# Performance work log

Hardware: AMD Instinct MI355X
Metric: run time of the kernel (lower is better)

Reference implementation:

```python
import jax, jax.numpy as jnp
import numpy as np

B, S, D_MODEL, N_HEADS = 4, 2048, 1024, 16
HEAD = D_MODEL // N_HEADS  # 64


def setup_inputs() -> dict:
    key = jax.random.key(0)
    ks = jax.random.split(key, 9)
    s = 1.0 / np.sqrt(D_MODEL)
    return {
        "query": jax.random.normal(ks[0], (B, S, D_MODEL), jnp.float32),
        "key_in": jax.random.normal(ks[1], (B, S, D_MODEL), jnp.float32),
        "value": jax.random.normal(ks[2], (B, S, D_MODEL), jnp.float32),
        "Wq": jax.random.normal(ks[3], (D_MODEL, D_MODEL), jnp.float32) * s,
        "bq": jnp.zeros((D_MODEL,), jnp.float32),
        "Wk": jax.random.normal(ks[4], (D_MODEL, D_MODEL), jnp.float32) * s,
        "bk": jnp.zeros((D_MODEL,), jnp.float32),
        "Wv": jax.random.normal(ks[5], (D_MODEL, D_MODEL), jnp.float32) * s,
        "bv": jnp.zeros((D_MODEL,), jnp.float32),
    }


def reference(query, key_in, value, Wq, bq, Wk, bk, Wv, bv):
    # Dense projections (Keras Dense: x @ W + b)
    q = query @ Wq + bq     # [B,S,D]
    k = key_in @ Wk + bk    # [B,S,D]
    v = value @ Wv + bv     # [B,S,D]
    # split heads -> [B,S,H,Dh]
    q = q.reshape(B, S, N_HEADS, HEAD)
    k = k.reshape(B, S, N_HEADS, HEAD)
    v = v.reshape(B, S, N_HEADS, HEAD)
    scale = 1.0 / jnp.sqrt(jnp.float32(HEAD))
    # full attention matrix [B,H,Sq,Sk] (faithful to original un-fused form)
    scores = jnp.einsum('bqhd,bkhd->bhqk', q, k) * scale
    alpha = jax.nn.softmax(scores, axis=-1)
    ctx = jnp.einsum('bhqk,bkhd->bqhd', alpha, v)  # [B,Sq,H,Dh]
    return ctx.reshape(B, S, D_MODEL)
```

## Files before the change

kernel.cpp:

```cpp
#include <hip/hip_runtime.h>
#include <hip/hip_bf16.h>

#define S_LEN 2048
#define DM    1024
#define NH    16
#define HD    64

typedef __attribute__((ext_vector_type(8))) short short8;
typedef __attribute__((ext_vector_type(4))) short short4v;
typedef __attribute__((ext_vector_type(4))) float f32x4;

__device__ __forceinline__ short f2bf(float f) {
    union { float f; unsigned u; } x; x.f = f;
    unsigned u = x.u;
    return (short)((u + 0x7FFFu + ((u >> 16) & 1u)) >> 16);
}
__device__ __forceinline__ short f2bf_ru(float f) {
    return (short)((__float_as_uint(f) + 0x8000u) >> 16);
}
__device__ __forceinline__ unsigned pk2bf(float a, float b) {
    unsigned ua = __float_as_uint(a) + 0x8000u;
    unsigned ub = __float_as_uint(b) + 0x8000u;
    return (ua >> 16) | (ub & 0xFFFF0000u);
}
__device__ __forceinline__ float fexp2(float x) {
#if __has_builtin(__builtin_amdgcn_exp2f)
    return __builtin_amdgcn_exp2f(x);
#else
    return exp2f(x);
#endif
}
__device__ __forceinline__ void gload_lds16(const void* g, void* l) {
    __builtin_amdgcn_global_load_lds(
        (const __attribute__((address_space(1))) unsigned int*)g,
        (__attribute__((address_space(3))) unsigned int*)l, 16, 0, 0);
}

__global__ void wt_kernel(const float* __restrict__ Wq, const float* __restrict__ Wk,
                          const float* __restrict__ Wv, short* __restrict__ wt_base) {
    __shared__ float t[32][33];
    const float* W = (blockIdx.z == 0) ? Wq : (blockIdx.z == 1 ? Wk : Wv);
    short* WT = wt_base + (size_t)blockIdx.z * DM * DM;
    int kb = blockIdx.x * 32, nb = blockIdx.y * 32;
    int tx = threadIdx.x, ty = threadIdx.y;
#pragma unroll
    for (int r = 0; r < 4; r++)
        t[ty + 8 * r][tx] = W[(size_t)(kb + ty + 8 * r) * DM + nb + tx];
    __syncthreads();
#pragma unroll
    for (int r = 0; r < 4; r++)
        WT[(size_t)(nb + ty + 8 * r) * DM + kb + tx] = f2bf(t[tx][ty + 8 * r]);
}

__global__ __launch_bounds__(512, 2) void projf_kernel(
        const float* __restrict__ Xq, const float* __restrict__ Xk,
        const float* __restrict__ Xv, const short* __restrict__ WT3,
        const float* __restrict__ bq, const float* __restrict__ bk,
        const float* __restrict__ bv,
        short* __restrict__ Qh, short* __restrict__ Kh, short* __restrict__ Vt,
        float qscale) {
    __shared__ __align__(16) short As[2][128 * 32];
    __shared__ __align__(16) short Bs[2][256 * 32];
    const int bid = blockIdx.x;
    const int swz = (bid & 7) * 96 + (bid >> 3);
    const int nx = swz & 3;
    const int my = (swz >> 2) & 63;
    const int z  = swz >> 8;

    const float* X = (z == 0) ? Xq : (z == 1) ? Xk : Xv;
    const short* WT = WT3 + (size_t)z * DM * DM;
    const float* bias = (z == 0) ? bq : (z == 1) ? bk : bv;
    short* out = (z == 0) ? Qh : (z == 1) ? Kh : Vt;
    const float scale = (z == 0) ? qscale : 1.0f;
    const int mode = (z == 2);

    const int tid = threadIdx.x;
    const int lane = tid & 63, w = tid >> 6;
    const int l15 = lane & 15, quad = lane >> 4;
    const int n0 = nx * 256, m0 = my * 128;
    const int wm = (w & 1) * 64, wn = (w >> 1) * 64;
    const int arow = tid >> 2;
    const int ako  = (tid & 3) * 8;

    const float* xb = X + (size_t)m0 * DM;

    f32x4 acc[4][4];
#pragma unroll
    for (int i = 0; i < 4; i++)
#pragma unroll
        for (int j = 0; j < 4; j++) { acc[i][j][0] = 0.f; acc[i][j][1] = 0.f; acc[i][j][2] = 0.f; acc[i][j][3] = 0.f; }

    auto stageB = [&](int k0, int bi) {
#pragma unroll
        for (int it = 0; it < 2; it++) {
            int c = it * 512 + tid;
            int row = c >> 2, ko = (c & 3) * 8;
            gload_lds16(WT + (size_t)(n0 + row) * DM + k0 + ko, Bs[bi] + c * 8);
        }
    };

    float4 a0, a1;
    a0 = *(const float4*)(xb + (size_t)arow * DM + ako);
    a1 = *(const float4*)(xb + (size_t)arow * DM + ako + 4);
    stageB(0, 0);
    {
        uint4 p;
        p.x = pk2bf(a0.x, a0.y); p.y = pk2bf(a0.z, a0.w);
        p.z = pk2bf(a1.x, a1.y); p.w = pk2bf(a1.z, a1.w);
        *(uint4*)(As[0] + arow * 32 + ako) = p;
    }

    for (int t = 0; t < 32; t++) {
        const int bi = t & 1;
        const int kn = t * 32 + 32;
        __syncthreads();

        short8 af[4], bf[4];
#pragma unroll
        for (int i = 0; i < 4; i++)
            af[i] = *(const short8*)(As[bi] + (wm + i * 16 + l15) * 32 + quad * 8);
#pragma unroll
        for (int j = 0; j < 4; j++)
            bf[j] = *(const short8*)(Bs[bi] + (wn + j * 16 + l15) * 32 + quad * 8);

        if (t < 31) {
            a0 = *(const float4*)(xb + (size_t)arow * DM + kn + ako);
            a1 = *(const float4*)(xb + (size_t)arow * DM + kn + ako + 4);
            stageB(kn, bi ^ 1);
        }

#pragma unroll
        for (int i = 0; i < 4; i++)
#pragma unroll
            for (int j = 0; j < 4; j++)
                acc[i][j] = __builtin_amdgcn_mfma_f32_16x16x32_bf16(af[i], bf[j], acc[i][j], 0, 0, 0);

        if (t < 31) {
            uint4 p;
            p.x = pk2bf(a0.x, a0.y); p.y = pk2bf(a0.z, a0.w);
            p.z = pk2bf(a1.x, a1.y); p.w = pk2bf(a1.z, a1.w);
            *(uint4*)(As[bi ^ 1] + arow * 32 + ako) = p;
        }
    }

#pragma unroll
    for (int j = 0; j < 4; j++) {
        int col = n0 + wn + j * 16 + l15;
        float bv_ = bias[col];
        int h = col >> 6, d = col & 63;
#pragma unroll
        for (int i = 0; i < 4; i++) {
            int rowbase = m0 + wm + i * 16 + quad * 4;
            int bb = rowbase >> 11, s0 = rowbase & 2047;
            if (mode == 0) {
#pragma unroll
                for (int r = 0; r < 4; r++)
                    out[((size_t)(bb * NH + h) * S_LEN + (s0 + r)) * HD + d] =
                        f2bf((acc[i][j][r] + bv_) * scale);
            } else {
                short4v pk;
#pragma unroll
                for (int r = 0; r < 4; r++) pk[r] = f2bf((acc[i][j][r] + bv_) * scale);
                *(short4v*)(out + ((size_t)(bb * NH + h) * HD + d) * S_LEN + s0) = pk;
            }
        }
    }
}

__global__ __launch_bounds__(256, 3) void attn_kernel(
        const short* __restrict__ Q, const short* __restrict__ K,
        const short* __restrict__ V, float* __restrict__ out) {
    __shared__ __align__(16) short Ks[2][2][64][32];
    __shared__ __align__(16) short Vs[2][2][64][32];
    __shared__ __align__(16) short ps[4][2][16 * 72];
    const int bid = blockIdx.x;
    const int swz = (bid & 7) * 128 + (bid >> 3);
    const int qi = swz & 15;
    const int h  = (swz >> 4) & 15;
    const int b  = swz >> 8;

    const int tid = threadIdx.x;
    const int lane = tid & 63, w = tid >> 6;
    const int l15 = lane & 15, quad = lane >> 4;
    const int q0 = qi * 128;
    const size_t bh = (size_t)(b * NH + h);
    const short* qp = Q + bh * S_LEN * HD;
    const short* kp = K + bh * S_LEN * HD;
    const short* vp = V + bh * (size_t)HD * S_LEN;

    short8 qa[2][2];
#pragma unroll
    for (int s = 0; s < 2; s++) {
        const short* qr = qp + (size_t)(q0 + w * 32 + s * 16 + l15) * HD + quad * 8;
        qa[s][0] = *(const short8*)(qr);
        qa[s][1] = *(const short8*)(qr + 32);
    }

    f32x4 o[2][4];
    float lsum[2][4];
#pragma unroll
    for (int s = 0; s < 2; s++)
#pragma unroll
        for (int d = 0; d < 4; d++) {
            o[s][d][0] = 0.f; o[s][d][1] = 0.f; o[s][d][2] = 0.f; o[s][d][3] = 0.f;
            lsum[s][d] = 0.f;
        }

    auto stageKV = [&](int kt, int bi) {
        short* kd = &Ks[bi][0][0][0];
        short* vd = &Vs[bi][0][0][0];
#pragma unroll
        for (int it = 0; it < 2; it++) {
            int c = it * 256 + tid;
            int half = c >> 8, row = (c >> 2) & 63, chunk = c & 3;
            int co = half * 32 + chunk * 8;
            gload_lds16(kp + (size_t)(kt + row) * HD + co, kd + c * 8);
            gload_lds16(vp + (size_t)row * S_LEN + kt + co, vd + c * 8);
        }
    };

    stageKV(0, 0);

    for (int t = 0; t < 32; t++) {
        const int bi = t & 1;
        __syncthreads();
        if (t < 31) stageKV((t + 1) << 6, bi ^ 1);

        short8 kf[4][2];
#pragma unroll
        for (int nb = 0; nb < 4; nb++) {
            kf[nb][0] = *(const short8*)(&Ks[bi][0][nb * 16 + l15][quad * 8]);
            kf[nb][1] = *(const short8*)(&Ks[bi][1][nb * 16 + l15][quad * 8]);
        }
        f32x4 sacc[2][4];
#pragma unroll
        for (int nb = 0; nb < 4; nb++)
#pragma unroll
            for (int s = 0; s < 2; s++) {
                f32x4 zz; zz[0] = 0.f; zz[1] = 0.f; zz[2] = 0.f; zz[3] = 0.f;
                zz = __builtin_amdgcn_mfma_f32_16x16x32_bf16(qa[s][0], kf[nb][0], zz, 0, 0, 0);
                sacc[s][nb] = __builtin_amdgcn_mfma_f32_16x16x32_bf16(qa[s][1], kf[nb][1], zz, 0, 0, 0);
            }
#pragma unroll
        for (int s = 0; s < 2; s++)
#pragma unroll
            for (int r = 0; r < 4; r++)
#pragma unroll
                for (int nb = 0; nb < 4; nb++) {
                    float p = fexp2(sacc[s][nb][r]);
                    lsum[s][r] += p;
                    ps[w][s][(quad * 4 + r) * 72 + nb * 16 + l15] = f2bf_ru(p);
                }
        asm volatile("s_waitcnt lgkmcnt(0)" ::: "memory");
        short8 pa[2][2];
#pragma unroll
        for (int s = 0; s < 2; s++) {
            pa[s][0] = *(const short8*)(&ps[w][s][l15 * 72 + quad * 8]);
            pa[s][1] = *(const short8*)(&ps[w][s][l15 * 72 + 32 + quad * 8]);
        }
#pragma unroll
        for (int dd = 0; dd < 4; dd++) {
            short8 v0 = *(const short8*)(&Vs[bi][0][dd * 16 + l15][quad * 8]);
            short8 v1 = *(const short8*)(&Vs[bi][1][dd * 16 + l15][quad * 8]);
#pragma unroll
            for (int s = 0; s < 2; s++) {
                o[s][dd] = __builtin_amdgcn_mfma_f32_16x16x32_bf16(pa[s][0], v0, o[s][dd], 0, 0, 0);
                o[s][dd] = __builtin_amdgcn_mfma_f32_16x16x32_bf16(pa[s][1], v1, o[s][dd], 0, 0, 0);
            }
        }
    }

#pragma unroll
    for (int s = 0; s < 2; s++) {
#pragma unroll
        for (int r = 0; r < 4; r++) {
            float l = lsum[s][r];
            l += __shfl_xor(l, 1);
            l += __shfl_xor(l, 2);
            l += __shfl_xor(l, 4);
            l += __shfl_xor(l, 8);
            lsum[s][r] = 1.f / l;
        }
        float* orow = out + ((size_t)b * S_LEN + q0 + w * 32 + s * 16 + quad * 4) * DM + h * HD + l15;
#pragma unroll
        for (int r = 0; r < 4; r++)
#pragma unroll
            for (int dd = 0; dd < 4; dd++)
                orow[(size_t)r * DM + dd * 16] = o[s][dd][r] * lsum[s][r];
    }
}

extern "C" void kernel_launch(void* const* d_in, const int* in_sizes, int n_in,
                              void* d_out, int out_size, void* d_ws, size_t ws_size,
                              hipStream_t stream) {
    const float* query  = (const float*)d_in[0];
    const float* key_in = (const float*)d_in[1];
    const float* value  = (const float*)d_in[2];
    const float* Wq = (const float*)d_in[3];
    const float* bq = (const float*)d_in[4];
    const float* Wk = (const float*)d_in[5];
    const float* bk = (const float*)d_in[6];
    const float* Wv = (const float*)d_in[7];
    const float* bv = (const float*)d_in[8];

    short* wt = (short*)d_ws;
    short* Qh = wt + 3 * 1048576;
    short* Kh = Qh + 8388608;
    short* Vt = Kh + 8388608;
    float* out = (float*)d_out;

    const float QSCALE = 0.125f * 1.44269504088896340736f;

    wt_kernel<<<dim3(32, 32, 3), dim3(32, 8), 0, stream>>>(Wq, Wk, Wv, wt);
    projf_kernel<<<dim3(768), 512, 0, stream>>>(query, key_in, value, wt,
                                                bq, bk, bv, Qh, Kh, Vt, QSCALE);
    attn_kernel<<<dim3(1024), 256, 0, stream>>>(Qh, Kh, Vt, out);
}
```

Measured before the change: 349.0 us.

## Transpose QK^T MFMA and pass probabilities via lane shuffles instead of LDS

```diff
diff --git a/kernel.cpp b/kernel.cpp
--- a/kernel.cpp
+++ b/kernel.cpp
@@ -115,19 +115,19 @@
         const int kn = t * 32 + 32;
         __syncthreads();
 
-        short8 af[4], bf[4];
-#pragma unroll
-        for (int i = 0; i < 4; i++)
-            af[i] = *(const short8*)(As[bi] + (wm + i * 16 + l15) * 32 + quad * 8);
-#pragma unroll
-        for (int j = 0; j < 4; j++)
-            bf[j] = *(const short8*)(Bs[bi] + (wn + j * 16 + l15) * 32 + quad * 8);
-
         if (t < 31) {
             a0 = *(const float4*)(xb + (size_t)arow * DM + kn + ako);
             a1 = *(const float4*)(xb + (size_t)arow * DM + kn + ako + 4);
             stageB(kn, bi ^ 1);
         }
+
+        short8 af[4], bf[4];
+#pragma unroll
+        for (int i = 0; i < 4; i++)
+            af[i] = *(const short8*)(As[bi] + (wm + i * 16 + l15) * 32 + quad * 8);
+#pragma unroll
+        for (int j = 0; j < 4; j++)
+            bf[j] = *(const short8*)(Bs[bi] + (wn + j * 16 + l15) * 32 + quad * 8);
 
 #pragma unroll
         for (int i = 0; i < 4; i++)
@@ -167,12 +167,11 @@
     }
 }
 
-__global__ __launch_bounds__(256, 3) void attn_kernel(
+__global__ __launch_bounds__(256, 4) void attn_kernel(
         const short* __restrict__ Q, const short* __restrict__ K,
         const short* __restrict__ V, float* __restrict__ out) {
     __shared__ __align__(16) short Ks[2][2][64][32];
     __shared__ __align__(16) short Vs[2][2][64][32];
-    __shared__ __align__(16) short ps[4][2][16 * 72];
     const int bid = blockIdx.x;
     const int swz = (bid & 7) * 128 + (bid >> 3);
     const int qi = swz & 15;
@@ -197,14 +196,16 @@
     }
 
     f32x4 o[2][4];
-    float lsum[2][4];
+    float lsum[2] = {0.f, 0.f};
 #pragma unroll
     for (int s = 0; s < 2; s++)
 #pragma unroll
         for (int d = 0; d < 4; d++) {
             o[s][d][0] = 0.f; o[s][d][1] = 0.f; o[s][d][2] = 0.f; o[s][d][3] = 0.f;
-            lsum[s][d] = 0.f;
-        }
+        }
+
+    const int srcLo = ((quad & 1) * 2) * 16 + l15;
+    const int srcHi = srcLo + 16;
 
     auto stageKV = [&](int kt, int bi) {
         short* kd = &Ks[bi][0][0][0];
@@ -238,26 +239,46 @@
 #pragma unroll
             for (int s = 0; s < 2; s++) {
                 f32x4 zz; zz[0] = 0.f; zz[1] = 0.f; zz[2] = 0.f; zz[3] = 0.f;
-                zz = __builtin_amdgcn_mfma_f32_16x16x32_bf16(qa[s][0], kf[nb][0], zz, 0, 0, 0);
-                sacc[s][nb] = __builtin_amdgcn_mfma_f32_16x16x32_bf16(qa[s][1], kf[nb][1], zz, 0, 0, 0);
-            }
+                zz = __builtin_amdgcn_mfma_f32_16x16x32_bf16(kf[nb][0], qa[s][0], zz, 0, 0, 0);
+                sacc[s][nb] = __builtin_amdgcn_mfma_f32_16x16x32_bf16(kf[nb][1], qa[s][1], zz, 0, 0, 0);
+            }
+
+        unsigned up[2][4][2];
 #pragma unroll
         for (int s = 0; s < 2; s++)
 #pragma unroll
-            for (int r = 0; r < 4; r++)
-#pragma unroll
-                for (int nb = 0; nb < 4; nb++) {
-                    float p = fexp2(sacc[s][nb][r]);
-                    lsum[s][r] += p;
-                    ps[w][s][(quad * 4 + r) * 72 + nb * 16 + l15] = f2bf_ru(p);
-                }
-        asm volatile("s_waitcnt lgkmcnt(0)" ::: "memory");
+            for (int nb = 0; nb < 4; nb++) {
+                float p0 = fexp2(sacc[s][nb][0]);
+                float p1 = fexp2(sacc[s][nb][1]);
+                float p2 = fexp2(sacc[s][nb][2]);
+                float p3 = fexp2(sacc[s][nb][3]);
+                lsum[s] += (p0 + p1) + (p2 + p3);
+                up[s][nb][0] = pk2bf(p0, p1);
+                up[s][nb][1] = pk2bf(p2, p3);
+            }
+
         short8 pa[2][2];
 #pragma unroll
-        for (int s = 0; s < 2; s++) {
-            pa[s][0] = *(const short8*)(&ps[w][s][l15 * 72 + quad * 8]);
-            pa[s][1] = *(const short8*)(&ps[w][s][l15 * 72 + 32 + quad * 8]);
-        }
+        for (int s = 0; s < 2; s++)
+#pragma unroll
+            for (int hf = 0; hf < 2; hf++) {
+                unsigned a0 = (unsigned)__shfl((int)up[s][2 * hf][0], srcLo);
+                unsigned a1 = (unsigned)__shfl((int)up[s][2 * hf][1], srcLo);
+                unsigned a2 = (unsigned)__shfl((int)up[s][2 * hf][0], srcHi);
+                unsigned a3 = (unsigned)__shfl((int)up[s][2 * hf][1], srcHi);
+                unsigned b0 = (unsigned)__shfl((int)up[s][2 * hf + 1][0], srcLo);
+                unsigned b1 = (unsigned)__shfl((int)up[s][2 * hf + 1][1], srcLo);
+                unsigned b2 = (unsigned)__shfl((int)up[s][2 * hf + 1][0], srcHi);
+                unsigned b3 = (unsigned)__shfl((int)up[s][2 * hf + 1][1], srcHi);
+                const bool hi = (quad >> 1) != 0;
+                uint4 uu;
+                uu.x = hi ? b0 : a0;
+                uu.y = hi ? b1 : a1;
+                uu.z = hi ? b2 : a2;
+                uu.w = hi ? b3 : a3;
+                pa[s][hf] = *(short8*)&uu;
+            }
+
 #pragma unroll
         for (int dd = 0; dd < 4; dd++) {
             short8 v0 = *(const short8*)(&Vs[bi][0][dd * 16 + l15][quad * 8]);
@@ -270,23 +291,26 @@
         }
     }
 
+    float inv[2];
 #pragma unroll
     for (int s = 0; s < 2; s++) {
-#pragma unroll
-        for (int r = 0; r < 4; r++) {
-            float l = lsum[s][r];
-            l += __shfl_xor(l, 1);
-            l += __shfl_xor(l, 2);
-            l += __shfl_xor(l, 4);
-            l += __shfl_xor(l, 8);
-            lsum[s][r] = 1.f / l;
-        }
+        float l = lsum[s];
+        l += __shfl_xor(l, 16);
+        l += __shfl_xor(l, 32);
+        inv[s] = 1.f / l;
+    }
+#pragma unroll
+    for (int s = 0; s < 2; s++) {
+        float ir[4];
+#pragma unroll
+        for (int r = 0; r < 4; r++)
+            ir[r] = __shfl(inv[s], quad * 4 + r);
         float* orow = out + ((size_t)b * S_LEN + q0 + w * 32 + s * 16 + quad * 4) * DM + h * HD + l15;
 #pragma unroll
         for (int r = 0; r < 4; r++)
 #pragma unroll
             for (int dd = 0; dd < 4; dd++)
-                orow[(size_t)r * DM + dd * 16] = o[s][dd][r] * lsum[s][r];
+                orow[(size_t)r * DM + dd * 16] = o[s][dd][r] * ir[r];
     }
 }
 
```

New measurement: 339.9 us. 1.03x faster.

## Load K/V fragments directly from global memory in attention, drop LDS staging

Applied to the files above, without the earlier changes.

```diff
diff --git a/kernel.cpp b/kernel.cpp
--- a/kernel.cpp
+++ b/kernel.cpp
@@ -115,19 +115,19 @@
         const int kn = t * 32 + 32;
         __syncthreads();
 
-        short8 af[4], bf[4];
-#pragma unroll
-        for (int i = 0; i < 4; i++)
-            af[i] = *(const short8*)(As[bi] + (wm + i * 16 + l15) * 32 + quad * 8);
-#pragma unroll
-        for (int j = 0; j < 4; j++)
-            bf[j] = *(const short8*)(Bs[bi] + (wn + j * 16 + l15) * 32 + quad * 8);
-
         if (t < 31) {
             a0 = *(const float4*)(xb + (size_t)arow * DM + kn + ako);
             a1 = *(const float4*)(xb + (size_t)arow * DM + kn + ako + 4);
             stageB(kn, bi ^ 1);
         }
+
+        short8 af[4], bf[4];
+#pragma unroll
+        for (int i = 0; i < 4; i++)
+            af[i] = *(const short8*)(As[bi] + (wm + i * 16 + l15) * 32 + quad * 8);
+#pragma unroll
+        for (int j = 0; j < 4; j++)
+            bf[j] = *(const short8*)(Bs[bi] + (wn + j * 16 + l15) * 32 + quad * 8);
 
 #pragma unroll
         for (int i = 0; i < 4; i++)
@@ -167,11 +167,9 @@
     }
 }
 
-__global__ __launch_bounds__(256, 3) void attn_kernel(
+__global__ __launch_bounds__(256, 4) void attn_kernel(
         const short* __restrict__ Q, const short* __restrict__ K,
         const short* __restrict__ V, float* __restrict__ out) {
-    __shared__ __align__(16) short Ks[2][2][64][32];
-    __shared__ __align__(16) short Vs[2][2][64][32];
     __shared__ __align__(16) short ps[4][2][16 * 72];
     const int bid = blockIdx.x;
     const int swz = (bid & 7) * 128 + (bid >> 3);
@@ -196,6 +194,9 @@
         qa[s][1] = *(const short8*)(qr + 32);
     }
 
+    const short* kbase0 = kp + (size_t)l15 * HD + quad * 8;
+    const short* vbase  = vp + (size_t)l15 * S_LEN + quad * 8;
+
     f32x4 o[2][4];
     float lsum[2][4];
 #pragma unroll
@@ -206,31 +207,15 @@
             lsum[s][d] = 0.f;
         }
 
-    auto stageKV = [&](int kt, int bi) {
-        short* kd = &Ks[bi][0][0][0];
-        short* vd = &Vs[bi][0][0][0];
-#pragma unroll
-        for (int it = 0; it < 2; it++) {
-            int c = it * 256 + tid;
-            int half = c >> 8, row = (c >> 2) & 63, chunk = c & 3;
-            int co = half * 32 + chunk * 8;
-            gload_lds16(kp + (size_t)(kt + row) * HD + co, kd + c * 8);
-            gload_lds16(vp + (size_t)row * S_LEN + kt + co, vd + c * 8);
-        }
-    };
-
-    stageKV(0, 0);
-
     for (int t = 0; t < 32; t++) {
-        const int bi = t & 1;
-        __syncthreads();
-        if (t < 31) stageKV((t + 1) << 6, bi ^ 1);
+        const int kt = t << 6;
 
         short8 kf[4][2];
 #pragma unroll
         for (int nb = 0; nb < 4; nb++) {
-            kf[nb][0] = *(const short8*)(&Ks[bi][0][nb * 16 + l15][quad * 8]);
-            kf[nb][1] = *(const short8*)(&Ks[bi][1][nb * 16 + l15][quad * 8]);
+            const short* kr = kbase0 + (size_t)(kt + nb * 16) * HD;
+            kf[nb][0] = *(const short8*)(kr);
+            kf[nb][1] = *(const short8*)(kr + 32);
         }
         f32x4 sacc[2][4];
 #pragma unroll
@@ -241,6 +226,15 @@
                 zz = __builtin_amdgcn_mfma_f32_16x16x32_bf16(qa[s][0], kf[nb][0], zz, 0, 0, 0);
                 sacc[s][nb] = __builtin_amdgcn_mfma_f32_16x16x32_bf16(qa[s][1], kf[nb][1], zz, 0, 0, 0);
             }
+
+        short8 vf[4][2];
+#pragma unroll
+        for (int dd = 0; dd < 4; dd++) {
+            const short* vr = vbase + (size_t)(dd * 16) * S_LEN + kt;
+            vf[dd][0] = *(const short8*)(vr);
+            vf[dd][1] = *(const short8*)(vr + 32);
+        }
+
 #pragma unroll
         for (int s = 0; s < 2; s++)
 #pragma unroll
@@ -258,16 +252,14 @@
             pa[s][0] = *(const short8*)(&ps[w][s][l15 * 72 + quad * 8]);
             pa[s][1] = *(const short8*)(&ps[w][s][l15 * 72 + 32 + quad * 8]);
         }
-#pragma unroll
-        for (int dd = 0; dd < 4; dd++) {
-            short8 v0 = *(const short8*)(&Vs[bi][0][dd * 16 + l15][quad * 8]);
-            short8 v1 = *(const short8*)(&Vs[bi][1][dd * 16 + l15][quad * 8]);
+
+#pragma unroll
+        for (int dd = 0; dd < 4; dd++)
 #pragma unroll
             for (int s = 0; s < 2; s++) {
-                o[s][dd] = __builtin_amdgcn_mfma_f32_16x16x32_bf16(pa[s][0], v0, o[s][dd], 0, 0, 0);
-                o[s][dd] = __builtin_amdgcn_mfma_f32_16x16x32_bf16(pa[s][1], v1, o[s][dd], 0, 0, 0);
+                o[s][dd] = __builtin_amdgcn_mfma_f32_16x16x32_bf16(pa[s][0], vf[dd][0], o[s][dd], 0, 0, 0);
+                o[s][dd] = __builtin_amdgcn_mfma_f32_16x16x32_bf16(pa[s][1], vf[dd][1], o[s][dd], 0, 0, 0);
             }
-        }
     }
 
 #pragma unroll
```

Result: slower. 474.4 us (+36.0%).

## Rework attention to 32x32 MFMA with register-resident P and swizzled LDS

Applied to the files above, without the earlier changes.

```diff
diff --git a/kernel.cpp b/kernel.cpp
--- a/kernel.cpp
+++ b/kernel.cpp
@@ -9,6 +9,7 @@
 typedef __attribute__((ext_vector_type(8))) short short8;
 typedef __attribute__((ext_vector_type(4))) short short4v;
 typedef __attribute__((ext_vector_type(4))) float f32x4;
+typedef __attribute__((ext_vector_type(16))) float f32x16;
 
 __device__ __forceinline__ short f2bf(float f) {
     union { float f; unsigned u; } x; x.f = f;
@@ -22,6 +23,11 @@
     unsigned ua = __float_as_uint(a) + 0x8000u;
     unsigned ub = __float_as_uint(b) + 0x8000u;
     return (ua >> 16) | (ub & 0xFFFF0000u);
+}
+__device__ __forceinline__ unsigned cvtpk(float a, float b) {
+    unsigned r;
+    asm("v_cvt_pk_bf16_f32 %0, %1, %2" : "=v"(r) : "v"(a), "v"(b));
+    return r;
 }
 __device__ __forceinline__ float fexp2(float x) {
 #if __has_builtin(__builtin_amdgcn_exp2f)
@@ -115,19 +121,19 @@
         const int kn = t * 32 + 32;
         __syncthreads();
 
-        short8 af[4], bf[4];
-#pragma unroll
-        for (int i = 0; i < 4; i++)
-            af[i] = *(const short8*)(As[bi] + (wm + i * 16 + l15) * 32 + quad * 8);
-#pragma unroll
-        for (int j = 0; j < 4; j++)
-            bf[j] = *(const short8*)(Bs[bi] + (wn + j * 16 + l15) * 32 + quad * 8);
-
         if (t < 31) {
             a0 = *(const float4*)(xb + (size_t)arow * DM + kn + ako);
             a1 = *(const float4*)(xb + (size_t)arow * DM + kn + ako + 4);
             stageB(kn, bi ^ 1);
         }
+
+        short8 af[4], bf[4];
+#pragma unroll
+        for (int i = 0; i < 4; i++)
+            af[i] = *(const short8*)(As[bi] + (wm + i * 16 + l15) * 32 + quad * 8);
+#pragma unroll
+        for (int j = 0; j < 4; j++)
+            bf[j] = *(const short8*)(Bs[bi] + (wn + j * 16 + l15) * 32 + quad * 8);
 
 #pragma unroll
         for (int i = 0; i < 4; i++)
@@ -167,12 +173,11 @@
     }
 }
 
-__global__ __launch_bounds__(256, 3) void attn_kernel(
+__global__ __launch_bounds__(256, 4) void attn_kernel(
         const short* __restrict__ Q, const short* __restrict__ K,
         const short* __restrict__ V, float* __restrict__ out) {
-    __shared__ __align__(16) short Ks[2][2][64][32];
-    __shared__ __align__(16) short Vs[2][2][64][32];
-    __shared__ __align__(16) short ps[4][2][16 * 72];
+    __shared__ __align__(16) short Ks[2][64][64];
+    __shared__ __align__(16) short Vs[2][64][64];
     const int bid = blockIdx.x;
     const int swz = (bid & 7) * 128 + (bid >> 3);
     const int qi = swz & 15;
@@ -181,41 +186,36 @@
 
     const int tid = threadIdx.x;
     const int lane = tid & 63, w = tid >> 6;
-    const int l15 = lane & 15, quad = lane >> 4;
+    const int l31 = lane & 31, hi = lane >> 5;
     const int q0 = qi * 128;
     const size_t bh = (size_t)(b * NH + h);
     const short* qp = Q + bh * S_LEN * HD;
     const short* kp = K + bh * S_LEN * HD;
     const short* vp = V + bh * (size_t)HD * S_LEN;
 
-    short8 qa[2][2];
-#pragma unroll
-    for (int s = 0; s < 2; s++) {
-        const short* qr = qp + (size_t)(q0 + w * 32 + s * 16 + l15) * HD + quad * 8;
-        qa[s][0] = *(const short8*)(qr);
-        qa[s][1] = *(const short8*)(qr + 32);
-    }
-
-    f32x4 o[2][4];
-    float lsum[2][4];
-#pragma unroll
-    for (int s = 0; s < 2; s++)
-#pragma unroll
-        for (int d = 0; d < 4; d++) {
-            o[s][d][0] = 0.f; o[s][d][1] = 0.f; o[s][d][2] = 0.f; o[s][d][3] = 0.f;
-            lsum[s][d] = 0.f;
-        }
+    short8 qa[4];
+    {
+        const short* qr = qp + (size_t)(q0 + w * 32 + l31) * HD + hi * 8;
+#pragma unroll
+        for (int ks = 0; ks < 4; ks++)
+            qa[ks] = *(const short8*)(qr + ks * 16);
+    }
+
+    f32x16 o[2];
+#pragma unroll
+    for (int db = 0; db < 2; db++)
+#pragma unroll
+        for (int i = 0; i < 16; i++) o[db][i] = 0.f;
+    float lsum = 0.f;
 
     auto stageKV = [&](int kt, int bi) {
-        short* kd = &Ks[bi][0][0][0];
-        short* vd = &Vs[bi][0][0][0];
 #pragma unroll
         for (int it = 0; it < 2; it++) {
             int c = it * 256 + tid;
-            int half = c >> 8, row = (c >> 2) & 63, chunk = c & 3;
-            int co = half * 32 + chunk * 8;
-            gload_lds16(kp + (size_t)(kt + row) * HD + co, kd + c * 8);
-            gload_lds16(vp + (size_t)row * S_LEN + kt + co, vd + c * 8);
+            int row = c >> 3, ch = c & 7;
+            int gc = ch ^ (row & 7);
+            gload_lds16(kp + (size_t)(kt + row) * HD + gc * 8, &Ks[bi][0][0] + c * 8);
+            gload_lds16(vp + (size_t)row * S_LEN + kt + gc * 8, &Vs[bi][0][0] + c * 8);
         }
     };
 
@@ -226,68 +226,64 @@
         __syncthreads();
         if (t < 31) stageKV((t + 1) << 6, bi ^ 1);
 
-        short8 kf[4][2];
-#pragma unroll
-        for (int nb = 0; nb < 4; nb++) {
-            kf[nb][0] = *(const short8*)(&Ks[bi][0][nb * 16 + l15][quad * 8]);
-            kf[nb][1] = *(const short8*)(&Ks[bi][1][nb * 16 + l15][quad * 8]);
-        }
-        f32x4 sacc[2][4];
-#pragma unroll
-        for (int nb = 0; nb < 4; nb++)
-#pragma unroll
-            for (int s = 0; s < 2; s++) {
-                f32x4 zz; zz[0] = 0.f; zz[1] = 0.f; zz[2] = 0.f; zz[3] = 0.f;
-                zz = __builtin_amdgcn_mfma_f32_16x16x32_bf16(qa[s][0], kf[nb][0], zz, 0, 0, 0);
-                sacc[s][nb] = __builtin_amdgcn_mfma_f32_16x16x32_bf16(qa[s][1], kf[nb][1], zz, 0, 0, 0);
+#pragma unroll
+        for (int kb = 0; kb < 2; kb++) {
+            const int krow = kb * 32 + l31;
+            short8 kf[4];
+#pragma unroll
+            for (int ks = 0; ks < 4; ks++)
+                kf[ks] = *(const short8*)(&Ks[bi][krow][((2 * ks + hi) ^ (krow & 7)) * 8]);
+            f32x16 s;
+#pragma unroll
+            for (int i = 0; i < 16; i++) s[i] = 0.f;
+            __builtin_amdgcn_s_setprio(1);
+#pragma unroll
+            for (int ks = 0; ks < 4; ks++)
+                s = __builtin_amdgcn_mfma_f32_32x32x16_bf16(kf[ks], qa[ks], s, 0, 0, 0);
+            __builtin_amdgcn_s_setprio(0);
+
+            float pe[16];
+#pragma unroll
+            for (int i = 0; i < 16; i++) { pe[i] = fexp2(s[i]); lsum += pe[i]; }
+
+#pragma unroll
+            for (int ksl = 0; ksl < 2; ksl++) {
+                const int ks = 2 * kb + ksl;
+                const int r0 = 8 * ksl;
+                unsigned c0 = cvtpk(pe[r0 + 0], pe[r0 + 1]);
+                unsigned c1 = cvtpk(pe[r0 + 2], pe[r0 + 3]);
+                unsigned c2 = cvtpk(pe[r0 + 4], pe[r0 + 5]);
+                unsigned c3 = cvtpk(pe[r0 + 6], pe[r0 + 7]);
+                asm volatile("v_permlane32_swap_b32 %0, %1" : "+v"(c0), "+v"(c2));
+                asm volatile("v_permlane32_swap_b32 %0, %1" : "+v"(c1), "+v"(c3));
+                uint4 uu; uu.x = c0; uu.y = c1; uu.z = c2; uu.w = c3;
+                short8 pb = *(short8*)&uu;
+                __builtin_amdgcn_s_setprio(1);
+#pragma unroll
+                for (int db = 0; db < 2; db++) {
+                    const int vrow = db * 32 + l31;
+                    short8 vf = *(const short8*)(&Vs[bi][vrow][((2 * ks + hi) ^ (vrow & 7)) * 8]);
+                    o[db] = __builtin_amdgcn_mfma_f32_32x32x16_bf16(vf, pb, o[db], 0, 0, 0);
+                }
+                __builtin_amdgcn_s_setprio(0);
             }
-#pragma unroll
-        for (int s = 0; s < 2; s++)
-#pragma unroll
-            for (int r = 0; r < 4; r++)
-#pragma unroll
-                for (int nb = 0; nb < 4; nb++) {
-                    float p = fexp2(sacc[s][nb][r]);
-                    lsum[s][r] += p;
-                    ps[w][s][(quad * 4 + r) * 72 + nb * 16 + l15] = f2bf_ru(p);
-                }
-        asm volatile("s_waitcnt lgkmcnt(0)" ::: "memory");
-        short8 pa[2][2];
-#pragma unroll
-        for (int s = 0; s < 2; s++) {
-            pa[s][0] = *(const short8*)(&ps[w][s][l15 * 72 + quad * 8]);
-            pa[s][1] = *(const short8*)(&ps[w][s][l15 * 72 + 32 + quad * 8]);
-        }
-#pragma unroll
-        for (int dd = 0; dd < 4; dd++) {
-            short8 v0 = *(const short8*)(&Vs[bi][0][dd * 16 + l15][quad * 8]);
-            short8 v1 = *(const short8*)(&Vs[bi][1][dd * 16 + l15][quad * 8]);
-#pragma unroll
-            for (int s = 0; s < 2; s++) {
-                o[s][dd] = __builtin_amdgcn_mfma_f32_16x16x32_bf16(pa[s][0], v0, o[s][dd], 0, 0, 0);
-                o[s][dd] = __builtin_amdgcn_mfma_f32_16x16x32_bf16(pa[s][1], v1, o[s][dd], 0, 0, 0);
-            }
-        }
-    }
-
-#pragma unroll
-    for (int s = 0; s < 2; s++) {
-#pragma unroll
-        for (int r = 0; r < 4; r++) {
-            float l = lsum[s][r];
-            l += __shfl_xor(l, 1);
-            l += __shfl_xor(l, 2);
-            l += __shfl_xor(l, 4);
-            l += __shfl_xor(l, 8);
-            lsum[s][r] = 1.f / l;
-        }
-        float* orow = out + ((size_t)b * S_LEN + q0 + w * 32 + s * 16 + quad * 4) * DM + h * HD + l15;
-#pragma unroll
-        for (int r = 0; r < 4; r++)
-#pragma unroll
-            for (int dd = 0; dd < 4; dd++)
-                orow[(size_t)r * DM + dd * 16] = o[s][dd][r] * lsum[s][r];
-    }
+        }
+    }
+
+    float l = lsum + __shfl_xor(lsum, 32);
+    float inv = 1.f / l;
+    float* orow = out + ((size_t)b * S_LEN + q0 + w * 32 + l31) * DM + h * HD + hi * 4;
+#pragma unroll
+    for (int db = 0; db < 2; db++)
+#pragma unroll
+        for (int g = 0; g < 4; g++) {
+            float4 v;
+            v.x = o[db][4 * g + 0] * inv;
+            v.y = o[db][4 * g + 1] * inv;
+            v.z = o[db][4 * g + 2] * inv;
+            v.w = o[db][4 * g + 3] * inv;
+            *(float4*)(orow + db * 32 + g * 8) = v;
+        }
 }
 
 extern "C" void kernel_launch(void* const* d_in, const int* in_sizes, int n_in,
```

New measurement: 314.4 us. -9.9%, faster.
